# Kernel optimization log

Measured on AMD Instinct MI355X. Metric: run time of the kernel, lower is better.

The kernel has to match this reference:

```python
import jax, jax.numpy as jnp
import numpy as np

BLANK = 0
SIZE_AVERAGE = True


def rnnt_loss(acts, labels, act_lens, label_lens):
    # acts: (B, T, U+1, V) raw logits; warp-transducer applies log_softmax internally
    B, T, U1, V = acts.shape
    U = U1 - 1
    logp = jax.nn.log_softmax(acts, axis=-1)          # (B,T,U1,V)
    lp_blank = logp[..., BLANK]                       # (B,T,U1)
    # emission log-prob of label u at grid point (t,u): logp[b,t,u,labels[b,u]]
    lp_emit = jnp.take_along_axis(
        logp[:, :, :U, :], labels[:, None, :, None].astype(jnp.int32), axis=3
    )[..., 0]                                         # (B,T,U)

    # alpha[0,0]=0 ; alpha[0,u] = sum_{k<u} emit[0,k]
    row0 = jnp.concatenate(
        [jnp.zeros((B, 1), acts.dtype), jnp.cumsum(lp_emit[:, 0, :], axis=1)], axis=1
    )                                                 # (B,U1)

    def outer(prev_row, xs):
        blank_prev, emit_t = xs                       # (B,U1), (B,U)
        fb = prev_row + blank_prev                    # arrive via blank from t-1
        def inner(carry, x):
            fb_u, em_prev = x                         # (B,), (B,)
            a = jnp.logaddexp(fb_u, carry + em_prev)  # blank vs emit path
            return a, a
        _, rest = jax.lax.scan(inner, fb[:, 0], (fb[:, 1:].T, emit_t.T))  # (U,B)
        row = jnp.concatenate([fb[:, :1], rest.T], axis=1)               # (B,U1)
        return row, row

    xs = (jnp.moveaxis(lp_blank[:, :-1, :], 1, 0),   # (T-1,B,U1)
          jnp.moveaxis(lp_emit[:, 1:, :], 1, 0))     # (T-1,B,U)
    _, rows = jax.lax.scan(outer, row0, xs)          # (T-1,B,U1)
    alpha = jnp.concatenate([row0[None], rows], axis=0)  # (T,B,U1)

    b_idx = jnp.arange(B)
    t_idx = act_lens.astype(jnp.int32) - 1
    u_idx = label_lens.astype(jnp.int32)
    loglike = alpha[t_idx, b_idx, u_idx] + lp_blank[b_idx, t_idx, u_idx]
    total = -jnp.sum(loglike)
    if SIZE_AVERAGE:
        total = total / B
    return total.reshape(1)


def setup_inputs() -> dict:
    key = jax.random.key(0)
    k1, k2, k3, k4 = jax.random.split(key, 4)
    B, T, U, V = 8, 256, 100, 128
    acts = jax.random.normal(k1, (B, T, U + 1, V), dtype=jnp.float32)
    labels = jax.random.randint(k2, (B, U), 0, V, dtype=jnp.int64)
    act_lens = jax.random.randint(k3, (B,), T // 2, T + 1, dtype=jnp.int32)
    label_lens = jax.random.randint(k4, (B,), U // 2, U + 1, dtype=jnp.int32)
    return {"acts": acts, "labels": labels, "act_lens": act_lens, "label_lens": label_lens}


def reference(acts, labels, act_lens, label_lens):
    return rnnt_loss(acts, labels, act_lens, label_lens)
```

## Files before the change

### kernel.cpp

```cpp
#include <hip/hip_runtime.h>
#include <math.h>


#define B_DIM  8
#define T_DIM  256
#define U_DIM  100
#define U1_DIM 101
#define V_DIM  128

#define ROWU   128
#define DROWS  360
#define NEGF   (-8.0e29f)
#define LOG2E  1.4426950408889634f
#define LN2    0.69314718055994530942f

#define NITMAX 88
#define VROWU  320
#define DEPTH  8

typedef unsigned uv2 __attribute__((ext_vector_type(2)));

__device__ __forceinline__ float ubit(unsigned u) { return __builtin_bit_cast(float, u); }
__device__ __forceinline__ float logadd2(float a, float b) {
    float m = fmaxf(a, b);
    float e = exp2f(-fabsf(a - b));
    return m + log2f(1.0f + e);
}
__device__ __forceinline__ float lse3(float a, float b, float c) {
    float m = fmaxf(fmaxf(a, b), c);
    float s = exp2f(a - m) + exp2f(b - m) + exp2f(c - m);
    return m + log2f(s);
}
__device__ __forceinline__ float lse5(float a, float b, float c, float d, float e) {
    float m = fmaxf(fmaxf(fmaxf(a, b), c), fmaxf(d, e));
    float s = exp2f(a - m) + exp2f(b - m) + exp2f(c - m) + exp2f(d - m) + exp2f(e - m);
    return m + log2f(s);
}
__device__ __forceinline__ float lane_shr1(float x) {
    int r = __builtin_amdgcn_update_dpp(0, __builtin_bit_cast(int, x),
                                        0x138 , 0xF, 0xF, true);
    return __builtin_bit_cast(float, r);
}
__device__ __forceinline__ unsigned f2bf(float f) {
    unsigned u = __builtin_bit_cast(unsigned, f);
    u += 0x7FFF + ((u >> 16) & 1);
    return u >> 16;
}

struct W2 { float tA, mA, lA, tB, mB, lB; };
__device__ __forceinline__ W2 buildW2m(uv2 c0, uv2 cm, int l, int d, int tl, int ul) {
    const int ua = 2 * l, ub = 2 * l + 1;
    float BL0a = ubit(c0.x << 16), EM0a = ubit(c0.x & 0xFFFF0000u);
    float BL0b = ubit(c0.y << 16), EM0b = ubit(c0.y & 0xFFFF0000u);
    float BLma = ubit(cm.x << 16), EMma = ubit(cm.x & 0xFFFF0000u);
    float BLmb = ubit(cm.y << 16), EMmb = ubit(cm.y & 0xFFFF0000u);
    BL0a = (ua <= ul && (unsigned)(d - 1 - ua) <= (unsigned)tl) ? BL0a : NEGF;
    BL0b = (ub <= ul && (unsigned)(d - 1 - ub) <= (unsigned)tl) ? BL0b : NEGF;
    EM0a = (ua >= 1 && ua <= ul && (unsigned)(d - ua) <= (unsigned)tl) ? EM0a : NEGF;
    EM0b = (ub <= ul && (unsigned)(d - ub) <= (unsigned)tl) ? EM0b : NEGF;
    BLma = (ua <= ul && (unsigned)(d - 2 - ua) <= (unsigned)tl) ? BLma : NEGF;
    BLmb = (ub <= ul && (unsigned)(d - 1 - ub) <= (unsigned)tl) ? BLmb : NEGF;
    EMma = (ua >= 1 && ua <= ul && (unsigned)(d - 1 - ua) <= (unsigned)tl) ? EMma : NEGF;
    EMmb = (ub <= ul && (unsigned)(d - 1 - ub) <= (unsigned)tl) ? EMmb : NEGF;
    float BLmp = lane_shr1(BLmb), EMmp = lane_shr1(EMmb);
    W2 w;
    w.tA = BLma + BL0a;
    w.mA = logadd2(EMma + BL0a, BLmp + EM0a);
    w.lA = EMmp + EM0a;
    w.tB = BLmb + BL0b;
    w.mB = logadd2(EMmb + BL0b, BLma + EM0b);
    w.lB = EMma + EM0b;
    if (l == 0) { w.mA = NEGF; w.lA = NEGF; w.lB = NEGF; }
    return w;
}

__device__ __forceinline__ void buildV4(const unsigned* combB, int dt, int l,
                                        int tl, int ul, float* out) {
    const unsigned* C = combB + (size_t)dt * ROWU + 2 * l;
    uv2 c0 = *(const uv2*)(C);
    uv2 c1 = *(const uv2*)(C - ROWU);
    uv2 c2 = *(const uv2*)(C - 2 * ROWU);
    uv2 c3 = *(const uv2*)(C - 3 * ROWU);
    W2 P = buildW2m(c0, c1, l, dt,     tl, ul);
    W2 Q = buildW2m(c2, c3, l, dt - 2, tl, ul);
    float Qt_b1 = lane_shr1(Q.tB), Qm_b1 = lane_shr1(Q.mB), Ql_b1 = lane_shr1(Q.lB);
    float Qt_a1 = lane_shr1(Q.tA), Qm_a1 = lane_shr1(Q.mA), Ql_a1 = lane_shr1(Q.lA);
    out[0] = P.tA + Q.tA;
    out[1] = logadd2(P.tA + Q.mA, P.mA + Qt_b1);
    out[2] = lse3(P.tA + Q.lA, P.mA + Qm_b1, P.lA + Qt_a1);
    out[3] = logadd2(P.mA + Ql_b1, P.lA + Qm_a1);
    out[4] = P.lA + Ql_a1;
    out[5] = P.tB + Q.tB;
    out[6] = logadd2(P.tB + Q.mB, P.mB + Q.tA);
    out[7] = lse3(P.tB + Q.lB, P.mB + Q.mA, P.lB + Qt_b1);
    out[8] = logadd2(P.mB + Q.lA, P.lB + Qm_b1);
    out[9] = P.lB + Ql_b1;
    if (l == 0) { out[1] = NEGF; out[2] = NEGF; out[3] = NEGF; out[4] = NEGF; }
}

__device__ __forceinline__ void prologue(const unsigned* combB, int start, int l,
                                         int tl, int ul, float& v0, float& v1) {
    v0 = (l == 0) ? 0.0f : NEGF;
    v1 = NEGF;
    for (int d = 1; d <= start; ++d) {
        uv2 c = *(const uv2*)(combB + (size_t)d * ROWU + 2 * l);
        const int ua = 2 * l, ub = 2 * l + 1;
        float bl0 = ubit(c.x << 16), em0 = ubit(c.x & 0xFFFF0000u);
        float bl1 = ubit(c.y << 16), em1 = ubit(c.y & 0xFFFF0000u);
        bl0 = (ua <= ul && (unsigned)(d - 1 - ua) <= (unsigned)tl) ? bl0 : NEGF;
        bl1 = (ub <= ul && (unsigned)(d - 1 - ub) <= (unsigned)tl) ? bl1 : NEGF;
        em0 = (ua >= 1 && ua <= ul && (unsigned)(d - ua) <= (unsigned)tl) ? em0 : NEGF;
        em1 = (ub <= ul && (unsigned)(d - ub) <= (unsigned)tl) ? em1 : NEGF;
        float left0 = lane_shr1(v1);
        float a0 = v0 + bl0, p0 = left0 + em0;
        float a1 = v1 + bl1, p1 = v0 + em1;
        v0 = logadd2(a0, p0);
        v1 = logadd2(a1, p1);
    }
}

__global__ __launch_bounds__(256) void lsm_kernel(
    const float* __restrict__ acts, const int* __restrict__ labels,
    const int* __restrict__ act_lens, const int* __restrict__ label_lens,
    unsigned short* __restrict__ comb, int* __restrict__ counter, int nrows)
{
    if (blockIdx.x == 0 && threadIdx.x == 0) *counter = 0;

    int rid = blockIdx.x * 8 + (threadIdx.x >> 5);
    if (rid >= nrows) return;
    int hl = threadIdx.x & 31;

    int u  = rid % U1_DIM;
    int bt = rid / U1_DIM;
    int b  = bt / T_DIM;
    int t  = bt - b * T_DIM;
    if (t >= act_lens[b] || u > label_lens[b]) return;

    const float* row = acts + (size_t)rid * V_DIM;
    float4 x = *reinterpret_cast<const float4*>(row + 4 * hl);
    float4 y = make_float4(x.x * LOG2E, x.y * LOG2E, x.z * LOG2E, x.w * LOG2E);

    float s = exp2f(y.x) + exp2f(y.y) + exp2f(y.z) + exp2f(y.w);
    #pragma unroll
    for (int off = 16; off; off >>= 1) s += __shfl_xor(s, off);
    float lse2 = log2f(s);

    unsigned short* C = comb + (size_t)b * DROWS * (ROWU * 2);
    int d = t + u + 1;
    if (hl == 0)
        C[(size_t)d * (ROWU * 2) + 2 * u] = (unsigned short)f2bf(y.x - lse2);
    if (u < U_DIM) {
        int lab = labels[b * U_DIM + u];
        if (hl == (lab >> 2)) {
            int r = lab & 3;
            float v = (r == 0) ? y.x : (r == 1) ? y.y : (r == 2) ? y.z : y.w;
            C[(size_t)d * (ROWU * 2) + 2 * u + 3] = (unsigned short)f2bf(v - lse2);
        }
    }
}

__global__ __launch_bounds__(512, 1) void dp2_kernel(
    const unsigned* __restrict__ comb,
    const int* __restrict__ act_lens, const int* __restrict__ label_lens,
    unsigned* __restrict__ V, float* __restrict__ loglike,
    int* __restrict__ counter, float* __restrict__ out)
{
    const int b = blockIdx.x;
    const int l = threadIdx.x & 63;
    const int w = threadIdx.x >> 6;

    const unsigned* combB = comb + (size_t)b * DROWS * ROWU;
    const int tl = act_lens[b] - 1;
    const int ul = label_lens[b];
    const int dfin  = tl + ul;
    const int start = dfin & 3;
    const int niter = dfin >> 2;
    unsigned* Vb = V + (size_t)b * NITMAX * VROWU;

    for (int it = w; it < niter; it += 8) {
        int dt = start + 4 * (it + 1);
        float o[10];
        buildV4(combB, dt, l, tl, ul, o);
        if (l < 52) {
            unsigned* ro = Vb + (size_t)it * VROWU;
            uv2 p0, p1, p2;
            p0.x = f2bf(o[0]) | (f2bf(o[1]) << 16); p0.y = f2bf(o[5]) | (f2bf(o[6]) << 16);
            p1.x = f2bf(o[2]) | (f2bf(o[3]) << 16); p1.y = f2bf(o[7]) | (f2bf(o[8]) << 16);
            p2.x = f2bf(o[4]);                      p2.y = f2bf(o[9]);
            *(uv2*)(ro + 2 * l)       = p0;
            *(uv2*)(ro + 104 + 2 * l) = p1;
            *(uv2*)(ro + 208 + 2 * l) = p2;
        }
    }
    __syncthreads();
    if (w != 0) return;

    float fin_bl = ubit(combB[(size_t)(dfin + 1) * ROWU + ul] << 16);
    float v0, v1;
    prologue(combB, start, l, tl, ul, v0, v1);
    float rf0 = NEGF, rf1 = NEGF;

    asm volatile("s_waitcnt vmcnt(0)" ::: "memory");

    const char* Vc = (const char*)Vb + 8 * l;
    uv2 r0[DEPTH], r1[DEPTH], r2[DEPTH];
    #pragma unroll
    for (int j = 0; j < DEPTH; ++j) {
        const char* p = Vc + (size_t)j * (VROWU * 4);
        asm volatile("global_load_dwordx2 %0, %1, off" : "=v"(r0[j]) : "v"(p));
        asm volatile("global_load_dwordx2 %0, %1, off" : "=v"(r1[j]) : "v"(p + 416));
        asm volatile("global_load_dwordx2 %0, %1, off" : "=v"(r2[j]) : "v"(p + 832));
    }
    const int ngroups = (niter + DEPTH - 1) / DEPTH;
    for (int g = 0; g < ngroups; ++g) {
        const int it0 = g * DEPTH;
        #pragma unroll
        for (int q = 0; q < 2; ++q) {
            asm volatile("s_waitcnt vmcnt(12)");
            __builtin_amdgcn_sched_barrier(0);
            #pragma unroll
            for (int j4 = 0; j4 < 4; ++j4) {
                const int J = q * 4 + j4;
                const int it = it0 + J;
                uv2 a0 = r0[J], a1 = r1[J], a2 = r2[J];
                float V0a = ubit(a0.x << 16), V1a = ubit(a0.x & 0xFFFF0000u);
                float V0b = ubit(a0.y << 16), V1b = ubit(a0.y & 0xFFFF0000u);
                float V2a = ubit(a1.x << 16), V3a = ubit(a1.x & 0xFFFF0000u);
                float V2b = ubit(a1.y << 16), V3b = ubit(a1.y & 0xFFFF0000u);
                float V4a = ubit(a2.x << 16), V4b = ubit(a2.y << 16);
                float s1 = lane_shr1(v1);
                float s0 = lane_shr1(v0);
                float s3 = lane_shr1(s1);
                float s2 = lane_shr1(s0);
                float nA = lse5(v0 + V0a, s1 + V1a, s0 + V2a, s3 + V3a, s2 + V4a);
                float nB = lse5(v1 + V0b, v0 + V1b, s1 + V2b, s0 + V3b, s3 + V4b);
                if (it == niter - 1) { rf0 = nA; rf1 = nB; }
                v0 = nA; v1 = nB;
                int rr = it + DEPTH; rr = rr < NITMAX ? rr : NITMAX - 1;
                const char* p = Vc + (size_t)rr * (VROWU * 4);
                asm volatile("global_load_dwordx2 %0, %1, off" : "=v"(r0[J]) : "v"(p));
                asm volatile("global_load_dwordx2 %0, %1, off" : "=v"(r1[J]) : "v"(p + 416));
                asm volatile("global_load_dwordx2 %0, %1, off" : "=v"(r2[J]) : "v"(p + 832));
            }
        }
    }

    float res = (ul & 1) ? rf1 : rf0;
    if (l == (ul >> 1)) {
        loglike[b] = LN2 * (res + fin_bl);
        __threadfence();
        int old = atomicAdd(counter, 1);
        if (old == B_DIM - 1) {
            __threadfence();
            float s = 0.0f;
            #pragma unroll
            for (int i = 0; i < B_DIM; ++i)
                s += __hip_atomic_load(&loglike[i], __ATOMIC_RELAXED,
                                       __HIP_MEMORY_SCOPE_AGENT);
            out[0] = -s / (float)B_DIM;
        }
    }
}

extern "C" void kernel_launch(void* const* d_in, const int* in_sizes, int n_in,
                              void* d_out, int out_size, void* d_ws, size_t ws_size,
                              hipStream_t stream) {
    const float* acts       = (const float*)d_in[0];
    const int*   labels     = (const int*)d_in[1];
    const int*   act_lens   = (const int*)d_in[2];
    const int*   label_lens = (const int*)d_in[3];

    unsigned* comb    = (unsigned*)d_ws;
    unsigned* V       = comb + (size_t)B_DIM * DROWS * ROWU;
    float*    loglike = (float*)(V + (size_t)B_DIM * NITMAX * VROWU);
    int*      counter = (int*)(loglike + B_DIM);

    int nrows   = B_DIM * T_DIM * U1_DIM;
    int nblocks = (nrows + 7) / 8;

    lsm_kernel<<<nblocks, 256, 0, stream>>>(acts, labels, act_lens, label_lens,
                                            (unsigned short*)comb, counter, nrows);
    dp2_kernel<<<B_DIM, 512, 0, stream>>>(comb, act_lens, label_lens,
                                          V, loglike, counter, (float*)d_out);
}
```

Baseline: 59.94 us.

## Split V-building into separate grid-wide kernel and deepen DP prefetch pipeline

```diff
diff --git a/kernel.cpp b/kernel.cpp
--- a/kernel.cpp
+++ b/kernel.cpp
@@ -16,7 +16,7 @@
 
 #define NITMAX 88
 #define VROWU  320
-#define DEPTH  8
+#define DEPTH  16
 
 typedef unsigned uv2 __attribute__((ext_vector_type(2)));
 
@@ -159,41 +159,53 @@
     }
 }
 
-__global__ __launch_bounds__(512, 1) void dp2_kernel(
+__global__ __launch_bounds__(256) void v4c_kernel(
     const unsigned* __restrict__ comb,
     const int* __restrict__ act_lens, const int* __restrict__ label_lens,
-    unsigned* __restrict__ V, float* __restrict__ loglike,
-    int* __restrict__ counter, float* __restrict__ out)
+    unsigned* __restrict__ V)
+{
+    int wid = blockIdx.x * 4 + (threadIdx.x >> 6);
+    if (wid >= B_DIM * NITMAX) return;
+    int l  = threadIdx.x & 63;
+    int b  = wid / NITMAX;
+    int it = wid - b * NITMAX;
+
+    int tl = act_lens[b] - 1, ul = label_lens[b];
+    int dfin = tl + ul, start = dfin & 3, niter = dfin >> 2;
+    if (it >= niter) return;
+    int dt = start + 4 * (it + 1);
+
+    float o[10];
+    buildV4(comb + (size_t)b * DROWS * ROWU, dt, l, tl, ul, o);
+
+    if (l < 52) {
+        unsigned* ro = V + (size_t)(b * NITMAX + it) * VROWU;
+        uv2 p0, p1, p2;
+        p0.x = f2bf(o[0]) | (f2bf(o[1]) << 16); p0.y = f2bf(o[5]) | (f2bf(o[6]) << 16);
+        p1.x = f2bf(o[2]) | (f2bf(o[3]) << 16); p1.y = f2bf(o[7]) | (f2bf(o[8]) << 16);
+        p2.x = f2bf(o[4]);                      p2.y = f2bf(o[9]);
+        __builtin_nontemporal_store(p0, (uv2*)(ro + 2 * l));
+        __builtin_nontemporal_store(p1, (uv2*)(ro + 104 + 2 * l));
+        __builtin_nontemporal_store(p2, (uv2*)(ro + 208 + 2 * l));
+    }
+}
+
+__global__ __launch_bounds__(64, 1) void dp3_kernel(
+    const unsigned* __restrict__ comb, const unsigned* __restrict__ V,
+    const int* __restrict__ act_lens, const int* __restrict__ label_lens,
+    float* __restrict__ loglike, int* __restrict__ counter,
+    float* __restrict__ out)
 {
     const int b = blockIdx.x;
-    const int l = threadIdx.x & 63;
-    const int w = threadIdx.x >> 6;
-
-    const unsigned* combB = comb + (size_t)b * DROWS * ROWU;
-    const int tl = act_lens[b] - 1;
-    const int ul = label_lens[b];
+    const int l = threadIdx.x;
+    const int tl    = act_lens[b] - 1;
+    const int ul    = label_lens[b];
     const int dfin  = tl + ul;
     const int start = dfin & 3;
     const int niter = dfin >> 2;
-    unsigned* Vb = V + (size_t)b * NITMAX * VROWU;
-
-    for (int it = w; it < niter; it += 8) {
-        int dt = start + 4 * (it + 1);
-        float o[10];
-        buildV4(combB, dt, l, tl, ul, o);
-        if (l < 52) {
-            unsigned* ro = Vb + (size_t)it * VROWU;
-            uv2 p0, p1, p2;
-            p0.x = f2bf(o[0]) | (f2bf(o[1]) << 16); p0.y = f2bf(o[5]) | (f2bf(o[6]) << 16);
-            p1.x = f2bf(o[2]) | (f2bf(o[3]) << 16); p1.y = f2bf(o[7]) | (f2bf(o[8]) << 16);
-            p2.x = f2bf(o[4]);                      p2.y = f2bf(o[9]);
-            *(uv2*)(ro + 2 * l)       = p0;
-            *(uv2*)(ro + 104 + 2 * l) = p1;
-            *(uv2*)(ro + 208 + 2 * l) = p2;
-        }
-    }
-    __syncthreads();
-    if (w != 0) return;
+
+    const unsigned* combB = comb + (size_t)b * DROWS * ROWU;
+    const char* Vc = (const char*)(V + (size_t)b * NITMAX * VROWU) + 8 * l;
 
     float fin_bl = ubit(combB[(size_t)(dfin + 1) * ROWU + ul] << 16);
     float v0, v1;
@@ -202,7 +214,6 @@
 
     asm volatile("s_waitcnt vmcnt(0)" ::: "memory");
 
-    const char* Vc = (const char*)Vb + 8 * l;
     uv2 r0[DEPTH], r1[DEPTH], r2[DEPTH];
     #pragma unroll
     for (int j = 0; j < DEPTH; ++j) {
@@ -215,8 +226,8 @@
     for (int g = 0; g < ngroups; ++g) {
         const int it0 = g * DEPTH;
         #pragma unroll
-        for (int q = 0; q < 2; ++q) {
-            asm volatile("s_waitcnt vmcnt(12)");
+        for (int q = 0; q < 4; ++q) {
+            asm volatile("s_waitcnt vmcnt(36)");
             __builtin_amdgcn_sched_barrier(0);
             #pragma unroll
             for (int j4 = 0; j4 < 4; ++j4) {
@@ -280,6 +291,8 @@
 
     lsm_kernel<<<nblocks, 256, 0, stream>>>(acts, labels, act_lens, label_lens,
                                             (unsigned short*)comb, counter, nrows);
-    dp2_kernel<<<B_DIM, 512, 0, stream>>>(comb, act_lens, label_lens,
-                                          V, loglike, counter, (float*)d_out);
-}
+    int vwaves = B_DIM * NITMAX;
+    v4c_kernel<<<(vwaves + 3) / 4, 256, 0, stream>>>(comb, act_lens, label_lens, V);
+    dp3_kernel<<<B_DIM, 64, 0, stream>>>(comb, V, act_lens, label_lens,
+                                         loglike, counter, (float*)d_out);
+}
```

After: 51.64 us. -13.9%, faster.
